# Kernel optimization log

Hardware: AMD Instinct MI355X
Metric: run time of the kernel (lower is better)

## Reference

```python
import jax, jax.numpy as jnp
import numpy as np

B, N, D = 1, 2048, 2048
H, DH, DR, MP = 16, 128, 64, 4
LOCAL = H * DH // MP  # per-shard qkv width
ATTN_MASK_VALUE = -1e10
LN_EPS = 1e-5


def setup_inputs() -> dict:
    key = jax.random.key(0)
    ks = jax.random.split(key, 5)
    s = 0.02
    return {
        "x": jax.random.normal(ks[0], (B, N, D), jnp.float32),
        "ln_scale": jnp.ones((D,), jnp.float32),
        "ln_offset": jnp.zeros((D,), jnp.float32),
        "w_qkv": jax.random.normal(ks[1], (D, 3 * H * DH), jnp.float32) * s,
        "w_attn_out": jax.random.normal(ks[2], (H * DH, D), jnp.float32) * s,
        "w_ff_in": jax.random.normal(ks[3], (D, 4 * D), jnp.float32) * s,
        "b_ff_in": jnp.zeros((4 * D,), jnp.float32),
        "w_ff_out": jax.random.normal(ks[4], (4 * D, D), jnp.float32) * s,
        "b_ff_out": jnp.zeros((D,), jnp.float32),
    }


def _rotate_every_two(x):
    # (..., d) -> interleaved (-x2, x1) pairs, GPT-J style
    x1 = x[..., ::2]
    x2 = x[..., 1::2]
    return jnp.stack((-x2, x1), axis=-1).reshape(x.shape)


def _fixed_pos_embedding(n, dim):
    inv_freq = 1.0 / (10000.0 ** (np.arange(0, dim, 2, dtype=np.float32) / dim))
    ang = np.einsum("i,j->ij", np.arange(n, dtype=np.float32), inv_freq)  # [n, dim/2]
    return jnp.asarray(np.sin(ang), jnp.float32), jnp.asarray(np.cos(ang), jnp.float32)


def _apply_rotary(x, sin, cos):
    # x: [b, n, h, d_rot]; sin/cos: [n, d_rot/2] repeated pairwise -> [1, n, 1, d_rot]
    sin = jnp.repeat(sin, 2, axis=-1)[None, :, None, :]
    cos = jnp.repeat(cos, 2, axis=-1)[None, :, None, :]
    return x * cos + _rotate_every_two(x) * sin


def reference(x, ln_scale, ln_offset, w_qkv, w_attn_out, w_ff_in, b_ff_in, w_ff_out, b_ff_out):
    # ---- LayerNorm (shared input to parallel attn + FFN) ----
    mu = jnp.mean(x, axis=-1, keepdims=True)
    var = jnp.var(x, axis=-1, keepdims=True)
    h = (x - mu) * jax.lax.rsqrt(var + LN_EPS) * ln_scale + ln_offset

    # ---- Causal self-attention with partial rotary ----
    qkv = (h @ w_qkv).reshape(B, N, MP, 3 * LOCAL)  # mp-sharded layout
    q, v, k = jnp.split(qkv, [LOCAL, 2 * LOCAL], axis=-1)
    heads = lambda t: t.reshape(B, N, H, DH)  # shard_heads: [b,n,mp,local] -> [b,n,h,dh]
    q, v, k = heads(q), heads(v), heads(k)

    sin, cos = _fixed_pos_embedding(N, DR)
    q = jnp.concatenate([_apply_rotary(q[..., :DR], sin, cos), q[..., DR:]], axis=-1)
    k = jnp.concatenate([_apply_rotary(k[..., :DR], sin, cos), k[..., DR:]], axis=-1)

    attn_scale = np.float32(np.sqrt(DH))
    logits = jnp.einsum("bihd,bjhd->bhij", q, k) / attn_scale
    causal_mask = jnp.triu(jnp.ones((N, N), dtype=bool), 1)
    logits = jnp.where(causal_mask, ATTN_MASK_VALUE, logits)
    attn_w = jax.nn.softmax(logits, axis=-1)
    attn_vec = jnp.einsum("bhij,bjhd->bihd", attn_w, v).reshape(B, N, H * DH)
    attn_out = attn_vec @ w_attn_out

    # ---- FFN (parallel branch, same LN input) ----
    ff_out = jax.nn.gelu(h @ w_ff_in + b_ff_in) @ w_ff_out + b_ff_out

    return attn_out + ff_out
```

## Files before the change

### kernel.cpp

```cpp
#include <hip/hip_runtime.h>
#include <hip/hip_bf16.h>

using bf16_t = __hip_bfloat16;
typedef __attribute__((ext_vector_type(8))) __bf16 bfrag;
typedef __attribute__((ext_vector_type(4))) float f32x4;

#define MFMA16(a, b, c) __builtin_amdgcn_mfma_f32_16x16x32_bf16((a), (b), (c), 0, 0, 0)

__device__ __forceinline__ void gload_lds16(const void* g, void* l) {
  __builtin_amdgcn_global_load_lds((const __attribute__((address_space(1))) void*)g,
                                   (__attribute__((address_space(3))) void*)l, 16, 0, 0);
}

__global__ __launch_bounds__(256) void transpose_cvt(const float* __restrict__ in,
    bf16_t* __restrict__ out, int K, int N) {
  __shared__ float t[32][33];
  const int n0 = blockIdx.x * 32, k0 = blockIdx.y * 32;
  const int tx = threadIdx.x & 31, ty = threadIdx.x >> 5;
#pragma unroll
  for (int i = 0; i < 4; ++i)
    t[ty + i * 8][tx] = in[(size_t)(k0 + ty + i * 8) * N + n0 + tx];
  __syncthreads();
#pragma unroll
  for (int i = 0; i < 4; ++i)
    out[(size_t)(n0 + ty + i * 8) * K + k0 + tx] = bf16_t(t[tx][ty + i * 8]);
}

__global__ __launch_bounds__(256) void ln_kernel(const float* __restrict__ x,
    const float* __restrict__ sc, const float* __restrict__ of, bf16_t* __restrict__ h) {
  __shared__ float red[8];
  const int n = blockIdx.x, tid = threadIdx.x;
  const float* xr = x + (size_t)n * 2048;
  float4 a = ((const float4*)xr)[tid * 2];
  float4 b = ((const float4*)xr)[tid * 2 + 1];
  float s = a.x + a.y + a.z + a.w + b.x + b.y + b.z + b.w;
  float q = a.x * a.x + a.y * a.y + a.z * a.z + a.w * a.w +
            b.x * b.x + b.y * b.y + b.z * b.z + b.w * b.w;
#pragma unroll
  for (int m = 32; m; m >>= 1) { s += __shfl_xor(s, m); q += __shfl_xor(q, m); }
  if ((tid & 63) == 0) { red[(tid >> 6) * 2] = s; red[(tid >> 6) * 2 + 1] = q; }
  __syncthreads();
  s = red[0] + red[2] + red[4] + red[6];
  q = red[1] + red[3] + red[5] + red[7];
  const float mu = s * (1.f / 2048.f);
  const float inv = rsqrtf(q * (1.f / 2048.f) - mu * mu + 1e-5f);
  const int base = tid * 8;
  float v[8] = {a.x, a.y, a.z, a.w, b.x, b.y, b.z, b.w};
  bf16_t* hr = h + (size_t)n * 2048 + base;
#pragma unroll
  for (int j = 0; j < 8; ++j) hr[j] = bf16_t((v[j] - mu) * inv * sc[base + j] + of[base + j]);
}

template <int EPI>
__global__ __launch_bounds__(512, 2) void gemm8p(
    const bf16_t* __restrict__ A, int lda, const bf16_t* __restrict__ BT, int ldb,
    const float* __restrict__ bias, float* __restrict__ Cf, bf16_t* __restrict__ Cb,
    int M, int N, int K, size_t splitStride) {
  extern __shared__ __align__(16) char lds[];
  const int tid = threadIdx.x, wid = tid >> 6, lane = tid & 63;
  const int lc = lane & 15, lg = lane >> 4;
  const int bm = blockIdx.y * 256, bn = blockIdx.x * 256;
  const int wr = wid >> 2, wc = wid & 3;
  const int NT = K >> 6;
  const int sr = wid * 16 + (lane >> 2);
  const int lgp = (lane & 3) ^ ((sr >> 1) & 3);
  const size_t rA = (size_t)128 * lda, rB = (size_t)128 * ldb;
  const bf16_t* pA0 = A + (size_t)blockIdx.z * K + (size_t)(bm + sr) * lda + lgp * 8;
  const bf16_t* pA1 = pA0 + 32;
  const bf16_t* pB0 = BT + (size_t)blockIdx.z * K + (size_t)(bn + sr) * ldb + lgp * 8;
  const bf16_t* pB1 = pB0 + 32;
  auto stA0 = [&](int ts) { char* b = lds + (((ts & 1) * 2 + 0) << 14) + wid * 1024;
    gload_lds16(pA0, b); gload_lds16(pA0 + rA, b + 8192); pA0 += 64; };
  auto stA1 = [&](int ts) { char* b = lds + (((ts & 1) * 2 + 1) << 14) + wid * 1024;
    gload_lds16(pA1, b); gload_lds16(pA1 + rA, b + 8192); pA1 += 64; };
  auto stB0 = [&](int ts) { char* b = lds + 65536 + (((ts & 1) * 2 + 0) << 14) + wid * 1024;
    gload_lds16(pB0, b); gload_lds16(pB0 + rB, b + 8192); pB0 += 64; };
  auto stB1 = [&](int ts) { char* b = lds + 65536 + (((ts & 1) * 2 + 1) << 14) + wid * 1024;
    gload_lds16(pB1, b); gload_lds16(pB1 + rB, b + 8192); pB1 += 64; };

  stA0(0); stB0(0); stA1(0); stB1(0); stA0(1); stB0(1); stA1(1);
  asm volatile("s_waitcnt vmcnt(6)" ::: "memory");
  __builtin_amdgcn_s_barrier();

  f32x4 acc[8][4] = {};
#define FR(off, row) \
  (*(const bfrag*)(lds + (off) + (row) * 64 + ((lg ^ (((row) >> 1) & 3)) << 4)))

  for (int t = 0; t < NT; ++t) {
    const int d = t & 1;
    const int aoff0 = (d * 2 + 0) << 14, aoff1 = (d * 2 + 1) << 14;
    const int boff0 = 65536 + aoff0, boff1 = 65536 + aoff1;
    bfrag a[8];
    {
#pragma unroll
      for (int m = 0; m < 8; ++m) a[m] = FR(aoff0, wr * 128 + m * 16 + lc);
      bfrag b0 = FR(boff0, wc * 64 + lc);
      bfrag b1 = FR(boff0, wc * 64 + 16 + lc);
      if (t + 1 < NT) stB1(t + 1);
      __builtin_amdgcn_s_barrier();
      asm volatile("s_waitcnt lgkmcnt(0)" ::: "memory");
      __builtin_amdgcn_sched_barrier(0);
      __builtin_amdgcn_s_setprio(1);
#pragma unroll
      for (int m = 0; m < 8; ++m) {
        acc[m][0] = MFMA16(a[m], b0, acc[m][0]);
        acc[m][1] = MFMA16(a[m], b1, acc[m][1]);
      }
      __builtin_amdgcn_s_setprio(0);
      __builtin_amdgcn_s_barrier();
    }
    {
      bfrag b2 = FR(boff0, wc * 64 + 32 + lc);
      bfrag b3 = FR(boff0, wc * 64 + 48 + lc);
      if (t + 2 < NT) stA0(t + 2);
      __builtin_amdgcn_s_barrier();
      asm volatile("s_waitcnt lgkmcnt(0)" ::: "memory");
      __builtin_amdgcn_sched_barrier(0);
      __builtin_amdgcn_s_setprio(1);
#pragma unroll
      for (int m = 0; m < 8; ++m) {
        acc[m][2] = MFMA16(a[m], b2, acc[m][2]);
        acc[m][3] = MFMA16(a[m], b3, acc[m][3]);
      }
      __builtin_amdgcn_s_setprio(0);
      __builtin_amdgcn_s_barrier();
    }
    {
#pragma unroll
      for (int m = 0; m < 8; ++m) a[m] = FR(aoff1, wr * 128 + m * 16 + lc);
      bfrag b0 = FR(boff1, wc * 64 + lc);
      bfrag b1 = FR(boff1, wc * 64 + 16 + lc);
      if (t + 2 < NT) stB0(t + 2);
      __builtin_amdgcn_s_barrier();
      asm volatile("s_waitcnt lgkmcnt(0)" ::: "memory");
      __builtin_amdgcn_sched_barrier(0);
      __builtin_amdgcn_s_setprio(1);
#pragma unroll
      for (int m = 0; m < 8; ++m) {
        acc[m][0] = MFMA16(a[m], b0, acc[m][0]);
        acc[m][1] = MFMA16(a[m], b1, acc[m][1]);
      }
      __builtin_amdgcn_s_setprio(0);
      __builtin_amdgcn_s_barrier();
    }
    {
      bfrag b2 = FR(boff1, wc * 64 + 32 + lc);
      bfrag b3 = FR(boff1, wc * 64 + 48 + lc);
      if (t + 2 < NT) stA1(t + 2);
      __builtin_amdgcn_s_barrier();
      asm volatile("s_waitcnt lgkmcnt(0)" ::: "memory");
      __builtin_amdgcn_sched_barrier(0);
      __builtin_amdgcn_s_setprio(1);
#pragma unroll
      for (int m = 0; m < 8; ++m) {
        acc[m][2] = MFMA16(a[m], b2, acc[m][2]);
        acc[m][3] = MFMA16(a[m], b3, acc[m][3]);
      }
      __builtin_amdgcn_s_setprio(0);
      if (t < NT - 2) asm volatile("s_waitcnt vmcnt(6)" ::: "memory");
      else            asm volatile("s_waitcnt vmcnt(0)" ::: "memory");
      __builtin_amdgcn_s_barrier();
    }
  }
#undef FR
  char* W = lds + wid * 16384;
  if (EPI & 8) {
    bf16_t* Wb = (bf16_t*)W;
#pragma unroll
    for (int mc = 0; mc < 2; ++mc) {
#pragma unroll
      for (int m4 = 0; m4 < 4; ++m4) {
#pragma unroll
        for (int n = 0; n < 4; ++n) {
          const int col = bn + wc * 64 + n * 16 + lc;
          float bv = (EPI & 1) ? bias[col] : 0.f;
#pragma unroll
          for (int i = 0; i < 4; ++i) {
            float v = acc[mc * 4 + m4][n][i];
            if (EPI & 1) v += bv;
            if (EPI & 2) v = 0.5f * v * (1.f + tanhf(0.7978845608028654f * (v + 0.044715f * v * v * v)));
            Wb[(m4 * 16 + lg * 4 + i) * 72 + n * 16 + lc] = bf16_t(v);
          }
        }
      }
      asm volatile("s_waitcnt lgkmcnt(0)" ::: "memory");
      __builtin_amdgcn_sched_barrier(0);
#pragma unroll
      for (int p = 0; p < 8; ++p) {
        const int rl = p * 8 + (lane >> 3), j = lane & 7;
        uint4 v = *(const uint4*)&Wb[rl * 72 + j * 8];
        const int grow = bm + wr * 128 + mc * 64 + rl;
        const int gcol = bn + wc * 64 + j * 8;
        *(uint4*)&Cb[(size_t)grow * N + gcol] = v;
      }
      asm volatile("s_waitcnt lgkmcnt(0)" ::: "memory");
      __builtin_amdgcn_sched_barrier(0);
    }
  } else {
    float* Wf = (float*)W;
    float* Cfz = Cf + (size_t)blockIdx.z * splitStride;
#pragma unroll
    for (int mc = 0; mc < 4; ++mc) {
#pragma unroll
      for (int m2 = 0; m2 < 2; ++m2) {
#pragma unroll
        for (int n = 0; n < 4; ++n) {
          const int col = bn + wc * 64 + n * 16 + lc;
          float bv = (EPI & 1) ? bias[col] : 0.f;
#pragma unroll
          for (int i = 0; i < 4; ++i) {
            float v = acc[mc * 2 + m2][n][i];
            if (EPI & 1) v += bv;
            if (EPI & 2) v = 0.5f * v * (1.f + tanhf(0.7978845608028654f * (v + 0.044715f * v * v * v)));
            Wf[(m2 * 16 + lg * 4 + i) * 72 + n * 16 + lc] = v;
          }
        }
      }
      asm volatile("s_waitcnt lgkmcnt(0)" ::: "memory");
      __builtin_amdgcn_sched_barrier(0);
#pragma unroll
      for (int p = 0; p < 8; ++p) {
        const int rl = p * 4 + (lane >> 4), j = lane & 15;
        float4 v = *(const float4*)&Wf[rl * 72 + j * 4];
        const int grow = bm + wr * 128 + mc * 32 + rl;
        const int gcol = bn + wc * 64 + j * 4;
        *(float4*)&Cfz[(size_t)grow * N + gcol] = v;
      }
      asm volatile("s_waitcnt lgkmcnt(0)" ::: "memory");
      __builtin_amdgcn_sched_barrier(0);
    }
  }
}

template <int NP, bool ADDIN, bool BIAS>
__global__ __launch_bounds__(256) void reduceP(const float* __restrict__ p0,
    const float* __restrict__ p1, const float* __restrict__ p2,
    const float* __restrict__ p3, const float* __restrict__ bias,
    float* __restrict__ out, int total, int colmask) {
  const int i = (blockIdx.x * 256 + threadIdx.x) * 4;
  if (i >= total) return;
  float4 v = *(const float4*)(p0 + i);
  float4 w = *(const float4*)(p1 + i);
  v.x += w.x; v.y += w.y; v.z += w.z; v.w += w.w;
  if (NP == 4) {
    float4 u = *(const float4*)(p2 + i);
    float4 z = *(const float4*)(p3 + i);
    v.x += u.x + z.x; v.y += u.y + z.y; v.z += u.z + z.z; v.w += u.w + z.w;
  }
  if (BIAS) {
    float4 b = *(const float4*)(bias + (i & colmask));
    v.x += b.x; v.y += b.y; v.z += b.z; v.w += b.w;
  }
  if (ADDIN) {
    float4 o = *(const float4*)(out + i);
    v.x += o.x; v.y += o.y; v.z += o.z; v.w += o.w;
  }
  *(float4*)(out + i) = v;
}

__global__ __launch_bounds__(128) void rope_kernel(const bf16_t* __restrict__ qkv,
    bf16_t* __restrict__ qh, bf16_t* __restrict__ kh, bf16_t* __restrict__ vT) {
  const int n = blockIdx.x, hh = blockIdx.y;
  const int d = threadIdx.x;
  const int mp = hh >> 2, hi = hh & 3;
  const bf16_t* row = qkv + (size_t)n * 6144 + mp * 1536 + hi * 128;
  float q = __bfloat162float(row[d]);
  float k = __bfloat162float(row[1024 + d]);
  if (d < 64) {
    const float ang = (float)n * powf(10000.f, -(float)(d & ~1) / 64.f);
    const float sn = sinf(ang), cs = cosf(ang);
    const float qp = __shfl_xor(q, 1), kp = __shfl_xor(k, 1);
    if (d & 1) { q = q * cs + qp * sn; k = k * cs + kp * sn; }
    else       { q = q * cs - qp * sn; k = k * cs - kp * sn; }
  }
  qh[((size_t)hh * 2048 + n) * 128 + d] = bf16_t(q * 0.08838834764831845f);
  kh[((size_t)hh * 2048 + n) * 128 + d] = bf16_t(k);
  vT[((size_t)hh * 128 + d) * 2048 + n] = row[512 + d];
}

__global__ __launch_bounds__(256) void attn_kernel(const bf16_t* __restrict__ qh,
    const bf16_t* __restrict__ kh, const bf16_t* __restrict__ vT, bf16_t* __restrict__ av) {
  __shared__ alignas(16) char Kbuf[2][16384];
  __shared__ alignas(16) char Vbuf[2][16384];
  __shared__ alignas(16) bf16_t Ps[4][16 * 72];
  const int p = blockIdx.x, h = blockIdx.y;
  const int tid = threadIdx.x, wid = tid >> 6, lane = tid & 63;
  const int lc = lane & 15, lg = lane >> 4;
  const int krow = wid * 4 + (lane >> 4);
  const int vrow = wid * 8 + (lane >> 3);

  auto stage = [&](int kv0, int d) {
#pragma unroll
    for (int i = 0; i < 4; ++i) {
      const int kr = i * 16 + krow;
      const int kch = (lane & 15) ^ (kr & 15);
      gload_lds16(kh + ((size_t)h * 2048 + kv0 + kr) * 128 + kch * 8,
                  Kbuf[d] + i * 4096 + wid * 1024);
      const int vr = i * 32 + vrow;
      const int vch = (lane & 7) ^ (vr & 7);
      gload_lds16(vT + ((size_t)h * 128 + vr) * 2048 + kv0 + vch * 8,
                  Vbuf[d] + i * 4096 + wid * 1024);
    }
  };
#define FRK(d, row, ch) (*(const bfrag*)(Kbuf[d] + (row) * 256 + (((ch) ^ ((row) & 15)) << 4)))
#define FRV(d, row, ch) (*(const bfrag*)(Vbuf[d] + (row) * 128 + (((ch) ^ ((row) & 7)) << 4)))

#pragma unroll 1
  for (int half = 0; half < 2; ++half) {
    const int qt = half ? (31 - p) : p;
    const int nkv = qt + 1;
    const int qr = qt * 64 + wid * 16;
    const bf16_t* Qb = qh + ((size_t)h * 2048 + qr) * 128;
    bfrag qf[4];
#pragma unroll
    for (int ks = 0; ks < 4; ++ks)
      qf[ks] = *(const bfrag*)&Qb[lc * 128 + ks * 32 + lg * 8];
    f32x4 O[8] = {};
    float mr[4] = {-1e30f, -1e30f, -1e30f, -1e30f};
    float lsum[4] = {0.f, 0.f, 0.f, 0.f};

    stage(0, 0);
    asm volatile("s_waitcnt vmcnt(0)" ::: "memory");
    __builtin_amdgcn_s_barrier();

#pragma unroll 1
    for (int kt = 0; kt < nkv; ++kt) {
      const int d = kt & 1;
      const int kv0 = kt * 64;
      if (kt + 1 < nkv) stage(kv0 + 64, d ^ 1);
      f32x4 s[4];
#pragma unroll
      for (int c = 0; c < 4; ++c) {
        f32x4 a = {};
#pragma unroll
        for (int ks = 0; ks < 4; ++ks) {
          bfrag kf = FRK(d, c * 16 + lc, ks * 4 + lg);
          a = MFMA16(qf[ks], kf, a);
        }
        s[c] = a;
      }
      if (kt == qt) {
#pragma unroll
        for (int c = 0; c < 4; ++c)
#pragma unroll
          for (int i = 0; i < 4; ++i)
            if (kv0 + c * 16 + lc > qr + lg * 4 + i) s[c][i] = -1e10f;
      }
      float pm[4];
#pragma unroll
      for (int i = 0; i < 4; ++i)
        pm[i] = fmaxf(fmaxf(s[0][i], s[1][i]), fmaxf(s[2][i], s[3][i]));
#pragma unroll
      for (int m = 1; m < 16; m <<= 1)
#pragma unroll
        for (int i = 0; i < 4; ++i) pm[i] = fmaxf(pm[i], __shfl_xor(pm[i], m));
      float al[4], rs[4];
#pragma unroll
      for (int i = 0; i < 4; ++i) {
        const float mn = fmaxf(mr[i], pm[i]);
        al[i] = __expf(mr[i] - mn);
        mr[i] = mn;
        rs[i] = 0.f;
      }
#pragma unroll
      for (int c = 0; c < 4; ++c)
#pragma unroll
        for (int i = 0; i < 4; ++i) {
          const float pv = __expf(s[c][i] - mr[i]);
          s[c][i] = pv; rs[i] += pv;
        }
#pragma unroll
      for (int m = 1; m < 16; m <<= 1)
#pragma unroll
        for (int i = 0; i < 4; ++i) rs[i] += __shfl_xor(rs[i], m);
#pragma unroll
      for (int i = 0; i < 4; ++i) lsum[i] = lsum[i] * al[i] + rs[i];
#pragma unroll
      for (int n = 0; n < 8; ++n)
#pragma unroll
        for (int i = 0; i < 4; ++i) O[n][i] *= al[i];
#pragma unroll
      for (int c = 0; c < 4; ++c)
#pragma unroll
        for (int i = 0; i < 4; ++i)
          Ps[wid][(lg * 4 + i) * 72 + c * 16 + lc] = bf16_t(s[c][i]);
#pragma unroll
      for (int k2 = 0; k2 < 2; ++k2) {
        bfrag pf = *(const bfrag*)((const char*)&Ps[wid][0] + lc * 144 + k2 * 64 + lg * 16);
#pragma unroll
        for (int n = 0; n < 8; ++n) {
          bfrag vf = FRV(d, n * 16 + lc, k2 * 4 + lg);
          O[n] = MFMA16(pf, vf, O[n]);
        }
      }
      if (kt + 1 < nkv) asm volatile("s_waitcnt vmcnt(0)" ::: "memory");
      asm volatile("s_waitcnt lgkmcnt(0)" ::: "memory");
      __builtin_amdgcn_s_barrier();
    }
#pragma unroll
    for (int n = 0; n < 8; ++n)
#pragma unroll
      for (int i = 0; i < 4; ++i)
        av[(size_t)(qr + lg * 4 + i) * 2048 + h * 128 + n * 16 + lc] = bf16_t(O[n][i] / lsum[i]);
    __builtin_amdgcn_s_barrier();
  }
#undef FRK
#undef FRV
}

extern "C" void kernel_launch(void* const* d_in, const int* in_sizes, int n_in,
                              void* d_out, int out_size, void* d_ws, size_t ws_size,
                              hipStream_t stream) {
  const float* x        = (const float*)d_in[0];
  const float* ln_scale = (const float*)d_in[1];
  const float* ln_offset= (const float*)d_in[2];
  const float* w_qkv    = (const float*)d_in[3];
  const float* w_ao     = (const float*)d_in[4];
  const float* w_ff_in  = (const float*)d_in[5];
  const float* b_ff_in  = (const float*)d_in[6];
  const float* w_ff_out = (const float*)d_in[7];
  const float* b_ff_out = (const float*)d_in[8];
  float* out = (float*)d_out;

  char* ws = (char*)d_ws;
  bf16_t* wqkvT   = (bf16_t*)(ws);
  bf16_t* waoT    = (bf16_t*)(ws + 25165824);
  bf16_t* wffinT  = (bf16_t*)(ws + 33554432);
  bf16_t* wffoutT = (bf16_t*)(ws + 67108864);
  bf16_t* h       = (bf16_t*)(ws + 100663296);
  bf16_t* qhb     = (bf16_t*)(ws + 109051904);
  bf16_t* khb     = (bf16_t*)(ws + 117440512);
  bf16_t* vTb     = (bf16_t*)(ws + 125829120);
  bf16_t* avb     = (bf16_t*)(ws + 134217728);
  bf16_t* qkvb    = (bf16_t*)(ws + 142606336);
  bf16_t* ff1b    = qkvb;
  float*  pa      = (float*)(ws + 142606336);
  float*  pf      = (float*)(ws);

  hipFuncSetAttribute((const void*)gemm8p<0>,  hipFuncAttributeMaxDynamicSharedMemorySize, 131072);
  hipFuncSetAttribute((const void*)gemm8p<8>,  hipFuncAttributeMaxDynamicSharedMemorySize, 131072);
  hipFuncSetAttribute((const void*)gemm8p<11>, hipFuncAttributeMaxDynamicSharedMemorySize, 131072);

  dim3 b256(256), b512(512);
  transpose_cvt<<<dim3(192, 64),  b256, 0, stream>>>(w_qkv,    wqkvT,   2048, 6144);
  transpose_cvt<<<dim3(64, 64),   b256, 0, stream>>>(w_ao,     waoT,    2048, 2048);
  transpose_cvt<<<dim3(256, 64),  b256, 0, stream>>>(w_ff_in,  wffinT,  2048, 8192);
  transpose_cvt<<<dim3(64, 256),  b256, 0, stream>>>(w_ff_out, wffoutT, 8192, 2048);
  ln_kernel<<<dim3(2048), b256, 0, stream>>>(x, ln_scale, ln_offset, h);

  gemm8p<8><<<dim3(24, 8, 1), b512, 131072, stream>>>(h, 2048, wqkvT, 2048,
      nullptr, nullptr, qkvb, 2048, 6144, 2048, 0);
  rope_kernel<<<dim3(2048, 16), dim3(128), 0, stream>>>(qkvb, qhb, khb, vTb);
  attn_kernel<<<dim3(16, 16), b256, 0, stream>>>(qhb, khb, vTb, avb);

  gemm8p<0><<<dim3(8, 8, 2), b512, 131072, stream>>>(avb, 2048, waoT, 2048,
      nullptr, pa, nullptr, 2048, 2048, 1024, (size_t)2048 * 2048);
  reduceP<2, false, false><<<dim3(4096), b256, 0, stream>>>(pa, pa + 4194304,
      nullptr, nullptr, nullptr, out, 4194304, 2047);

  gemm8p<11><<<dim3(32, 8, 1), b512, 131072, stream>>>(h, 2048, wffinT, 2048,
      b_ff_in, nullptr, ff1b, 2048, 8192, 2048, 0);

  gemm8p<0><<<dim3(8, 8, 4), b512, 131072, stream>>>(ff1b, 8192, wffoutT, 8192,
      nullptr, pf, nullptr, 2048, 2048, 2048, (size_t)2048 * 2048);
  reduceP<4, true, true><<<dim3(4096), b256, 0, stream>>>(pf, pf + 4194304,
      pf + 2 * 4194304, pf + 3 * 4194304, b_ff_out, out, 4194304, 2047);
}
```

Before: 452.2 us.

## Split attention KV range three ways and merge partials in a combine kernel

The causal attention kernel now launches a third grid dimension, so each query tile's KV range is divided into three contiguous chunks. Each chunk writes an unnormalized bf16 output together with its per-row max and sum. A new combine kernel rescales and merges the three partials into the attention output. This triples the number of workgroups so the GPU's CUs are better occupied, at the cost of extra partial-result traffic, one more launch, and an additional bf16 rounding of the unnormalized partials.

```diff
diff --git a/kernel.cpp b/kernel.cpp
--- a/kernel.cpp
+++ b/kernel.cpp
@@ -279,11 +279,12 @@
 }
 
 __global__ __launch_bounds__(256) void attn_kernel(const bf16_t* __restrict__ qh,
-    const bf16_t* __restrict__ kh, const bf16_t* __restrict__ vT, bf16_t* __restrict__ av) {
+    const bf16_t* __restrict__ kh, const bf16_t* __restrict__ vT,
+    bf16_t* __restrict__ Op, float2* __restrict__ ml) {
   __shared__ alignas(16) char Kbuf[2][16384];
   __shared__ alignas(16) char Vbuf[2][16384];
   __shared__ alignas(16) bf16_t Ps[4][16 * 72];
-  const int p = blockIdx.x, h = blockIdx.y;
+  const int p = blockIdx.x, h = blockIdx.y, z = blockIdx.z;
   const int tid = threadIdx.x, wid = tid >> 6, lane = tid & 63;
   const int lc = lane & 15, lg = lane >> 4;
   const int krow = wid * 4 + (lane >> 4);
@@ -309,6 +310,8 @@
   for (int half = 0; half < 2; ++half) {
     const int qt = half ? (31 - p) : p;
     const int nkv = qt + 1;
+    const int lo = (z * nkv) / 3, hi = ((z + 1) * nkv) / 3;
+    const int nj = hi - lo;
     const int qr = qt * 64 + wid * 16;
     const bf16_t* Qb = qh + ((size_t)h * 2048 + qr) * 128;
     bfrag qf[4];
@@ -319,15 +322,16 @@
     float mr[4] = {-1e30f, -1e30f, -1e30f, -1e30f};
     float lsum[4] = {0.f, 0.f, 0.f, 0.f};
 
-    stage(0, 0);
-    asm volatile("s_waitcnt vmcnt(0)" ::: "memory");
-    __builtin_amdgcn_s_barrier();
-
+    if (nj > 0) {
+      stage(lo * 64, 0);
+      asm volatile("s_waitcnt vmcnt(0)" ::: "memory");
+      __builtin_amdgcn_s_barrier();
+    }
 #pragma unroll 1
-    for (int kt = 0; kt < nkv; ++kt) {
-      const int d = kt & 1;
+    for (int j = 0; j < nj; ++j) {
+      const int kt = lo + j, d = j & 1;
       const int kv0 = kt * 64;
-      if (kt + 1 < nkv) stage(kv0 + 64, d ^ 1);
+      if (j + 1 < nj) stage(kv0 + 64, d ^ 1);
       f32x4 s[4];
 #pragma unroll
       for (int c = 0; c < 4; ++c) {
@@ -393,19 +397,55 @@
           O[n] = MFMA16(pf, vf, O[n]);
         }
       }
-      if (kt + 1 < nkv) asm volatile("s_waitcnt vmcnt(0)" ::: "memory");
-      asm volatile("s_waitcnt lgkmcnt(0)" ::: "memory");
-      __builtin_amdgcn_s_barrier();
-    }
+      if (j + 1 < nj) asm volatile("s_waitcnt vmcnt(0)" ::: "memory");
+      asm volatile("s_waitcnt lgkmcnt(0)" ::: "memory");
+      __builtin_amdgcn_s_barrier();
+    }
+    const size_t rb = (size_t)(z * 16 + h) * 2048 + qr;
 #pragma unroll
     for (int n = 0; n < 8; ++n)
 #pragma unroll
       for (int i = 0; i < 4; ++i)
-        av[(size_t)(qr + lg * 4 + i) * 2048 + h * 128 + n * 16 + lc] = bf16_t(O[n][i] / lsum[i]);
+        Op[(rb + lg * 4 + i) * 128 + n * 16 + lc] = bf16_t(O[n][i]);
+    if (lc == 0) {
+#pragma unroll
+      for (int i = 0; i < 4; ++i)
+        ml[rb + lg * 4 + i] = make_float2(mr[i], lsum[i]);
+    }
     __builtin_amdgcn_s_barrier();
   }
 #undef FRK
 #undef FRV
+}
+
+__global__ __launch_bounds__(256) void attn_combine(const bf16_t* __restrict__ Op,
+    const float2* __restrict__ ml, bf16_t* __restrict__ av) {
+  const int idx = blockIdx.x * 256 + threadIdx.x;
+  const int t = idx & 15, hr = idx >> 4;
+  const int ZS = 16 * 2048;
+  const size_t ZO = (size_t)ZS * 128;
+  const float2 m0 = ml[hr], m1 = ml[ZS + hr], m2 = ml[2 * ZS + hr];
+  const float M = fmaxf(fmaxf(m0.x, m1.x), m2.x);
+  const float w0 = __expf(m0.x - M), w1 = __expf(m1.x - M), w2 = __expf(m2.x - M);
+  const float inv = 1.f / (w0 * m0.y + w1 * m1.y + w2 * m2.y);
+  const bf16_t* p0 = Op + (size_t)hr * 128 + t * 8;
+  uint4 a0 = *(const uint4*)p0;
+  uint4 a1 = *(const uint4*)(p0 + ZO);
+  uint4 a2 = *(const uint4*)(p0 + 2 * ZO);
+  const unsigned* u0 = (const unsigned*)&a0;
+  const unsigned* u1 = (const unsigned*)&a1;
+  const unsigned* u2 = (const unsigned*)&a2;
+  bf16_t ov[8];
+#pragma unroll
+  for (int j = 0; j < 8; ++j) {
+    const int w = j >> 1, sh = (j & 1) * 16;
+    const float f0 = __uint_as_float(((u0[w] >> sh) & 0xffffu) << 16);
+    const float f1 = __uint_as_float(((u1[w] >> sh) & 0xffffu) << 16);
+    const float f2 = __uint_as_float(((u2[w] >> sh) & 0xffffu) << 16);
+    ov[j] = bf16_t((w0 * f0 + w1 * f1 + w2 * f2) * inv);
+  }
+  const int row = hr & 2047, hh = hr >> 11;
+  *(uint4*)(av + (size_t)row * 2048 + hh * 128 + t * 8) = *(const uint4*)ov;
 }
 
 extern "C" void kernel_launch(void* const* d_in, const int* in_sizes, int n_in,
@@ -436,6 +476,8 @@
   bf16_t* ff1b    = qkvb;
   float*  pa      = (float*)(ws + 142606336);
   float*  pf      = (float*)(ws);
+  bf16_t* Opart   = (bf16_t*)(ws);
+  float2* mlpart  = (float2*)(ws + 142606336 + 25165824);
 
   hipFuncSetAttribute((const void*)gemm8p<0>,  hipFuncAttributeMaxDynamicSharedMemorySize, 131072);
   hipFuncSetAttribute((const void*)gemm8p<8>,  hipFuncAttributeMaxDynamicSharedMemorySize, 131072);
@@ -451,7 +493,9 @@
   gemm8p<8><<<dim3(24, 8, 1), b512, 131072, stream>>>(h, 2048, wqkvT, 2048,
       nullptr, nullptr, qkvb, 2048, 6144, 2048, 0);
   rope_kernel<<<dim3(2048, 16), dim3(128), 0, stream>>>(qkvb, qhb, khb, vTb);
-  attn_kernel<<<dim3(16, 16), b256, 0, stream>>>(qhb, khb, vTb, avb);
+
+  attn_kernel<<<dim3(16, 16, 3), b256, 0, stream>>>(qhb, khb, vTb, Opart, mlpart);
+  attn_combine<<<dim3(2048), b256, 0, stream>>>(Opart, mlpart, avb);
 
   gemm8p<0><<<dim3(8, 8, 2), b512, 131072, stream>>>(avb, 2048, waoT, 2048,
       nullptr, pa, nullptr, 2048, 2048, 1024, (size_t)2048 * 2048);
```

After: 437.3 us. 1.03x faster.
